# Kernel tuning notes

Hardware: AMD Instinct MI355X
Metric: run time of the kernel (lower is better)

## Reference

```python
import jax, jax.numpy as jnp
import numpy as np

N_NODES = 50000
N_EDGES = 800000
D_IN = 64
D_HID = 256
BN_EPS = 1e-5


def setup_inputs() -> dict:
    key = jax.random.key(0)
    ks = jax.random.split(key, 8)
    s = 1.0 / np.sqrt(D_IN)
    sg = 1.0 / np.sqrt(D_HID)
    return {
        "xs": jax.random.normal(ks[0], (N_NODES, D_IN), jnp.float32),
        "edge_index": jax.random.randint(ks[1], (2, N_EDGES), 0, N_NODES, jnp.int64),
        "W_gcn": jax.random.normal(ks[2], (D_IN, D_HID), jnp.float32) * s,
        "b_gcn": jnp.zeros((D_HID,), jnp.float32),
        "W_lin": jax.random.normal(ks[3], (D_IN, D_HID), jnp.float32) * s,
        "b_lin": jnp.zeros((D_HID,), jnp.float32),
        "W_gate": jax.random.normal(ks[4], (D_HID, D_HID), jnp.float32) * sg,
        "b_gate": jnp.zeros((D_HID,), jnp.float32),
        "bn_gamma": jnp.ones((D_HID,), jnp.float32),
        "bn_beta": jnp.zeros((D_HID,), jnp.float32),
    }


def reference(xs, edge_index, W_gcn, b_gcn, W_lin, b_lin, W_gate, b_gate, bn_gamma, bn_beta):
    N = xs.shape[0]
    # --- GCNConv: add self loops, symmetric normalization D^-1/2 (A+I) D^-1/2 ---
    loops = jnp.arange(N, dtype=edge_index.dtype)
    src = jnp.concatenate([edge_index[0], loops])  # message sources
    dst = jnp.concatenate([edge_index[1], loops])  # aggregation targets
    deg = jax.ops.segment_sum(jnp.ones(src.shape, jnp.float32), dst, num_segments=N)
    dinv = jax.lax.rsqrt(jnp.maximum(deg, 1.0))  # deg >= 1 due to self loops
    norm = dinv[src] * dinv[dst]                 # [E+N]
    h = xs @ W_gcn                               # [N, D_HID]
    z = jax.ops.segment_sum(h[src] * norm[:, None], dst, num_segments=N) + b_gcn
    z = jnp.tanh(z)
    # --- gating + linear residual ---
    g = jax.nn.sigmoid(z @ W_gate + b_gate)
    xl = xs @ W_lin + b_lin
    out = jax.nn.relu((1.0 - g) * xl + g * z)
    # --- BatchNorm over nodes (training-mode batch statistics) ---
    mu = out.mean(axis=0)
    var = out.var(axis=0)
    out = (out - mu) * jax.lax.rsqrt(var + BN_EPS) * bn_gamma + bn_beta
    # dropout is identity in eval mode
    return out
```

## Files before the change

### kernel.cpp

```cpp
#include <hip/hip_runtime.h>
#include <math.h>

#define NN 50000
#define NE 800000
#define D_IN 64
#define D_HID 256
#define BN_EPS 1e-5f
#define ZSTR 264
#define SB 128
#define BCAP 64
#define BINCAP 8192

typedef __attribute__((ext_vector_type(8))) short short8;
typedef __attribute__((ext_vector_type(4))) float f32x4;
typedef __attribute__((ext_vector_type(4))) int int4v;
typedef __attribute__((ext_vector_type(4))) float float4v;

static __device__ __forceinline__ unsigned short f2bf(float f) {
    unsigned int u = __builtin_bit_cast(unsigned int, f);
    u += 0x7FFFu + ((u >> 16) & 1u);
    return (unsigned short)(u >> 16);
}
static __device__ __forceinline__ float bf2f(unsigned short s) {
    unsigned int u = ((unsigned int)s) << 16;
    return __builtin_bit_cast(float, u);
}
static __device__ __forceinline__ float fast_sigmoid(float x) {
    return __builtin_amdgcn_rcpf(1.0f + __expf(-x));
}
static __device__ __forceinline__ float fast_tanh(float x) {
    return 1.0f - 2.0f * __builtin_amdgcn_rcpf(__expf(2.0f * x) + 1.0f);
}

static __device__ __forceinline__ long a_addr(int i, int k) {
    return ((long)((i >> 4) * 2 + (k >> 5)) << 9) + ((((k >> 3) & 3) * 16 + (i & 15)) << 3) + (k & 7);
}

__global__ __launch_bounds__(256) void k_pre(const float* __restrict__ W_gcn,
                      const float* __restrict__ W_lin, const float* __restrict__ W_gate,
                      unsigned short* __restrict__ Wp_gcn, unsigned short* __restrict__ Wp_lin,
                      unsigned short* __restrict__ Wp_gate,
                      const int* __restrict__ eidx, int* __restrict__ bincur,
                      unsigned int* __restrict__ binbuf, int E) {
    int idx = blockIdx.x * blockDim.x + threadIdx.x;
    if (idx < 98304) {
        const float* W;
        unsigned short* Wp;
        int KC, o;
        if (idx < 16384)      { W = W_gcn;  Wp = Wp_gcn;  KC = 2; o = idx; }
        else if (idx < 32768) { W = W_lin;  Wp = Wp_lin;  KC = 2; o = idx - 16384; }
        else                  { W = W_gate; Wp = Wp_gate; KC = 8; o = idx - 32768; }
        int j = o & 7;
        int lane = (o >> 3) & 63;
        int rest = o >> 9;
        int kc = rest % KC;
        int ct = rest / KC;
        int col = ct * 16 + (lane & 15);
        int k = kc * 32 + (lane >> 4) * 8 + j;
        Wp[o] = f2bf(W[k * D_HID + col]);
    }

    int b = blockIdx.x;
    int t = threadIdx.x;
    int nbb = (E + 4095) >> 12;
    if (b < nbb) {
        __shared__ int bcnt[256];
        __shared__ int gbase[256];
        bcnt[t] = 0;
        __syncthreads();
        unsigned int pair[4][4];
        int bin[4][4], lr[4][4];
        bool val[4];
#pragma unroll
        for (int c = 0; c < 4; c++) {
            int e0 = b * 4096 + c * 1024 + t * 4;
            val[c] = e0 < E;
            if (val[c]) {
                int4v s = __builtin_nontemporal_load((const int4v*)(eidx + e0));
                int4v d = __builtin_nontemporal_load((const int4v*)(eidx + E + e0));
                int ss[4] = {s[0], s[1], s[2], s[3]};
                int dd[4] = {d[0], d[1], d[2], d[3]};
#pragma unroll
                for (int j = 0; j < 4; j++) {
                    int bi = dd[j] >> 8;
                    bin[c][j] = bi;
                    pair[c][j] = ((unsigned int)(dd[j] & 255) << 16) | (unsigned int)ss[j];
                    lr[c][j] = atomicAdd(&bcnt[bi], 1);
                }
            }
        }
        __syncthreads();
        if (bcnt[t] > 0) gbase[t] = atomicAdd(&bincur[t], bcnt[t]);
        __syncthreads();
#pragma unroll
        for (int c = 0; c < 4; c++)
            if (val[c]) {
#pragma unroll
                for (int j = 0; j < 4; j++) {
                    int slot = gbase[bin[c][j]] + lr[c][j];
                    if (slot < BINCAP)
                        binbuf[((long)bin[c][j] << 13) + slot] = pair[c][j];
                }
            }
    }
}

__global__ __launch_bounds__(256) void k_binfill(const unsigned int* __restrict__ binbuf,
                      const int* __restrict__ bincur, const float* __restrict__ xs,
                      unsigned short* __restrict__ csr, int* __restrict__ cnt,
                      float* __restrict__ dinv, unsigned short* __restrict__ xscaled,
                      unsigned short* __restrict__ xs_p, int n) {
    __shared__ unsigned short buck[256 * BCAP];
    __shared__ int lcnt[256];
    int b = blockIdx.x;
    int t = threadIdx.x;
    lcnt[t] = 0;
    __syncthreads();
    int tot = bincur[b];
    tot = tot < BINCAP ? tot : BINCAP;
    for (int i = t; i < tot; i += 256) {
        unsigned int p = binbuf[((long)b << 13) + i];
        int dl = p >> 16;
        int src = p & 0xFFFF;
        int r = atomicAdd(&lcnt[dl], 1);
        if (r < BCAP) buck[dl * BCAP + r] = (unsigned short)src;
    }
    __syncthreads();
    int node0 = b << 8;
    if (node0 + t < n) cnt[node0 + t] = lcnt[t];
#pragma unroll
    for (int v = 0; v < 8; v++) {
        int e = (v * 256 + t) * 8;
        int node = e >> 6;
        if (node0 + node < n)
            *(short8*)(csr + ((long)(node0 + node) << 6) + (e & 63)) = *(const short8*)(&buck[e]);
    }
#pragma unroll
    for (int v = 0; v < 8; v++) {
        int item = v * 256 + t;
        int nl = item >> 3;
        int sub = item & 7;
        int node = node0 + nl;
        if (node < n) {
            float dv = rsqrtf(1.0f + (float)lcnt[nl]);
            if (sub == 0) dinv[node] = dv;
            const float* p = xs + (long)node * D_IN + sub * 8;
            float4v f0 = __builtin_nontemporal_load((const float4v*)p);
            float4v f1 = __builtin_nontemporal_load((const float4v*)(p + 4));
            float vals[8] = {f0[0], f0[1], f0[2], f0[3], f1[0], f1[1], f1[2], f1[3]};
            short8 xsc, xsb;
#pragma unroll
            for (int j = 0; j < 8; j++) {
                xsc[j] = (short)f2bf(vals[j] * dv);
                xsb[j] = (short)f2bf(vals[j]);
            }
            *(short8*)(xscaled + (long)node * D_IN + sub * 8) = xsc;
            *(short8*)(xs_p + a_addr(node, sub * 8)) = xsb;
        } else if (node == n) {
            short8 zv = (short8){0, 0, 0, 0, 0, 0, 0, 0};
            *(short8*)(xscaled + (long)n * D_IN + sub * 8) = zv;
        }
    }
}

__global__ __launch_bounds__(256) void k_gather(const unsigned short* __restrict__ csr,
                                                const int* __restrict__ cnt,
                                                const unsigned short* __restrict__ xscaled,
                                                const float* __restrict__ dinv,
                                                unsigned short* __restrict__ agg_p, int n) {
    int wv = threadIdx.x >> 6;
    int lane = threadIdx.x & 63;
    int sub = lane & 7;
    int grp = lane >> 3;
    int i = blockIdx.x * 4 + wv;
    if (i >= n) return;
    int c = cnt[i];
    c = c < BCAP ? c : BCAP;
    float acc[8];
#pragma unroll
    for (int j = 0; j < 8; j++) acc[j] = 0.f;
    int idxv = (lane < c) ? (int)csr[((long)i << 6) + lane] : 0;
    int tmax = (c + 7) >> 3;
    for (int t = 0; t < tmax; t++) {
        int e = t * 8 + grp;
        int rowv = __shfl(idxv, e);
        int row = (e < c) ? rowv : n;
        short8 v = *(const short8*)(xscaled + (long)row * D_IN + sub * 8);
#pragma unroll
        for (int j = 0; j < 8; j++) acc[j] += bf2f((unsigned short)v[j]);
    }
#pragma unroll
    for (int d = 8; d <= 32; d <<= 1)
#pragma unroll
        for (int j = 0; j < 8; j++) acc[j] += __shfl_xor(acc[j], d);
    if (grp == 0) {
        float dv = dinv[i];
        short8 sv = *(const short8*)(xscaled + (long)i * D_IN + sub * 8);
        short8 o;
#pragma unroll
        for (int j = 0; j < 8; j++)
            o[j] = (short)f2bf((acc[j] + bf2f((unsigned short)sv[j])) * dv);
        *(short8*)(agg_p + a_addr(i, sub * 8)) = o;
    }
}

__global__ __launch_bounds__(256) void k_fused(const unsigned short* __restrict__ agg_p,
                        const unsigned short* __restrict__ xs_p,
                        const unsigned short* __restrict__ Wp_gcn,
                        const unsigned short* __restrict__ Wp_lin,
                        const unsigned short* __restrict__ Wp_gate,
                        const float* __restrict__ b_gcn,
                        const float* __restrict__ bg,
                        const float* __restrict__ bl,
                        unsigned short* __restrict__ out_pre,
                        int n) {
    __shared__ unsigned short z_lds[32 * ZSTR];

    int tid = threadIdx.x;
    int wv = tid >> 6;
    int lane = tid & 63;
    int l15 = lane & 15;
    int quad = lane >> 4;
    int rt0 = blockIdx.x * 2;

    short8 aggf[2][2], xsf[2][2];
#pragma unroll
    for (int r = 0; r < 2; r++)
#pragma unroll
        for (int kc = 0; kc < 2; kc++) {
            aggf[r][kc] = *(const short8*)(agg_p + ((long)((rt0 + r) * 2 + kc) << 9) + lane * 8);
            xsf[r][kc]  = *(const short8*)(xs_p  + ((long)((rt0 + r) * 2 + kc) << 9) + lane * 8);
        }

    {
        short8 wg[2][4];
#pragma unroll
        for (int kc = 0; kc < 2; kc++)
#pragma unroll
            for (int tn = 0; tn < 4; tn++)
                wg[kc][tn] = *(const short8*)(Wp_gcn + ((long)((wv * 4 + tn) * 2 + kc) << 9) + lane * 8);
        float bias[4];
#pragma unroll
        for (int tn = 0; tn < 4; tn++) bias[tn] = b_gcn[wv * 64 + tn * 16 + l15];
#pragma unroll
        for (int r = 0; r < 2; r++) {
            f32x4 accz[4];
#pragma unroll
            for (int c = 0; c < 4; c++) accz[c] = (f32x4){0.f, 0.f, 0.f, 0.f};
#pragma unroll
            for (int kc = 0; kc < 2; kc++)
#pragma unroll
                for (int tn = 0; tn < 4; tn++)
                    accz[tn] = __builtin_amdgcn_mfma_f32_16x16x32_bf16(aggf[r][kc], wg[kc][tn], accz[tn], 0, 0, 0);
#pragma unroll
            for (int tn = 0; tn < 4; tn++) {
                int col = wv * 64 + tn * 16 + l15;
#pragma unroll
                for (int r2 = 0; r2 < 4; r2++)
                    z_lds[(r * 16 + quad * 4 + r2) * ZSTR + col] = f2bf(fast_tanh(accz[tn][r2] + bias[tn]));
            }
        }
    }
    __syncthreads();

    uint2 o_pk[2][4];
    float bgc[4], blc[4];
#pragma unroll
    for (int tn = 0; tn < 4; tn++) {
        int col = wv * 64 + tn * 16 + l15;
        bgc[tn] = bg[col];
        blc[tn] = bl[col];
    }
#pragma unroll
    for (int tnp = 0; tnp < 2; tnp++) {
        f32x4 accl[2][2];
#pragma unroll
        for (int r = 0; r < 2; r++)
#pragma unroll
            for (int h = 0; h < 2; h++) accl[r][h] = (f32x4){0.f, 0.f, 0.f, 0.f};
#pragma unroll
        for (int kc = 0; kc < 2; kc++) {
            short8 wl0 = *(const short8*)(Wp_lin + ((long)((wv * 4 + tnp * 2 + 0) * 2 + kc) << 9) + lane * 8);
            short8 wl1 = *(const short8*)(Wp_lin + ((long)((wv * 4 + tnp * 2 + 1) * 2 + kc) << 9) + lane * 8);
#pragma unroll
            for (int r = 0; r < 2; r++) {
                accl[r][0] = __builtin_amdgcn_mfma_f32_16x16x32_bf16(xsf[r][kc], wl0, accl[r][0], 0, 0, 0);
                accl[r][1] = __builtin_amdgcn_mfma_f32_16x16x32_bf16(xsf[r][kc], wl1, accl[r][1], 0, 0, 0);
            }
        }
        f32x4 acc1[2][2];
#pragma unroll
        for (int r = 0; r < 2; r++)
#pragma unroll
            for (int h = 0; h < 2; h++) acc1[r][h] = (f32x4){0.f, 0.f, 0.f, 0.f};
#pragma unroll
        for (int kc = 0; kc < 8; kc++) {
            short8 w0 = *(const short8*)(Wp_gate + ((long)((wv * 4 + tnp * 2 + 0) * 8 + kc) << 9) + lane * 8);
            short8 w1 = *(const short8*)(Wp_gate + ((long)((wv * 4 + tnp * 2 + 1) * 8 + kc) << 9) + lane * 8);
#pragma unroll
            for (int r = 0; r < 2; r++) {
                short8 af = *(const short8*)(&z_lds[(r * 16 + l15) * ZSTR + kc * 32 + quad * 8]);
                acc1[r][0] = __builtin_amdgcn_mfma_f32_16x16x32_bf16(af, w0, acc1[r][0], 0, 0, 0);
                acc1[r][1] = __builtin_amdgcn_mfma_f32_16x16x32_bf16(af, w1, acc1[r][1], 0, 0, 0);
            }
        }
#pragma unroll
        for (int h = 0; h < 2; h++) {
            int tn = tnp * 2 + h;
            int col = wv * 64 + tn * 16 + l15;
#pragma unroll
            for (int r = 0; r < 2; r++) {
                unsigned short op4[4];
#pragma unroll
                for (int r2 = 0; r2 < 4; r2++) {
                    int rl = r * 16 + quad * 4 + r2;
                    float g = fast_sigmoid(acc1[r][h][r2] + bgc[tn]);
                    float zv = bf2f(z_lds[rl * ZSTR + col]);
                    float xv = accl[r][h][r2] + blc[tn];
                    float o = fmaxf((1.f - g) * xv + g * zv, 0.f);
                    op4[r2] = f2bf(o);
                }
                o_pk[r][tn].x = (unsigned int)op4[0] | ((unsigned int)op4[1] << 16);
                o_pk[r][tn].y = (unsigned int)op4[2] | ((unsigned int)op4[3] << 16);
            }
        }
    }
    __syncthreads();

#pragma unroll
    for (int r = 0; r < 2; r++)
#pragma unroll
        for (int tn = 0; tn < 4; tn++) {
            int col = wv * 64 + tn * 16 + l15;
            int rl = r * 16 + quad * 4;
            z_lds[(rl + 0) * ZSTR + col] = (unsigned short)(o_pk[r][tn].x & 0xFFFF);
            z_lds[(rl + 1) * ZSTR + col] = (unsigned short)(o_pk[r][tn].x >> 16);
            z_lds[(rl + 2) * ZSTR + col] = (unsigned short)(o_pk[r][tn].y & 0xFFFF);
            z_lds[(rl + 3) * ZSTR + col] = (unsigned short)(o_pk[r][tn].y >> 16);
        }
    __syncthreads();

#pragma unroll
    for (int it = 0; it < 4; it++) {
        int g = it * 2048 + tid * 8;
        int row = g >> 8;
        int col = g & 255;
        short8 v = *(const short8*)(&z_lds[row * ZSTR + col]);
        *(short8*)(out_pre + (long)(blockIdx.x * 32 + row) * D_HID + col) = v;
    }
    (void)n;
}

__global__ __launch_bounds__(256) void k_stats(const unsigned short* __restrict__ op,
                        float* __restrict__ colsum, float* __restrict__ colsumsq, int n) {
    __shared__ float reds[4][32][8];
    __shared__ float redq[4][32][8];
    int tid = threadIdx.x;
    int wv = tid >> 6;
    int lane = tid & 63;
    int cg = tid & 31;
    int rb = tid >> 5;
    float ls[8], lq[8];
#pragma unroll
    for (int j = 0; j < 8; j++) { ls[j] = 0.f; lq[j] = 0.f; }
    for (int row = blockIdx.x * 8 + rb; row < n; row += SB * 8) {
        short8 v = *(const short8*)(op + (long)row * D_HID + cg * 8);
#pragma unroll
        for (int j = 0; j < 8; j++) {
            float f = bf2f((unsigned short)v[j]);
            ls[j] += f;
            lq[j] += f * f;
        }
    }
#pragma unroll
    for (int j = 0; j < 8; j++) {
        ls[j] += __shfl_xor(ls[j], 32);
        lq[j] += __shfl_xor(lq[j], 32);
    }
    if (lane < 32) {
#pragma unroll
        for (int j = 0; j < 8; j++) {
            reds[wv][cg][j] = ls[j];
            redq[wv][cg][j] = lq[j];
        }
    }
    __syncthreads();
    if (wv == 0 && lane < 32) {
#pragma unroll
        for (int j = 0; j < 8; j++) {
            float s = reds[0][cg][j] + reds[1][cg][j] + reds[2][cg][j] + reds[3][cg][j];
            float q = redq[0][cg][j] + redq[1][cg][j] + redq[2][cg][j] + redq[3][cg][j];
            atomicAdd(&colsum[cg * 8 + j], s);
            atomicAdd(&colsumsq[cg * 8 + j], q);
        }
    }
}

__global__ __launch_bounds__(256) void k_bn_apply(const unsigned short* __restrict__ op,
                           float* __restrict__ out,
                           const float* __restrict__ colsum, const float* __restrict__ colsumsq,
                           const float* __restrict__ gamma, const float* __restrict__ beta,
                           int n, int total8) {
    int i8 = blockIdx.x * blockDim.x + threadIdx.x;
    if (i8 >= total8) return;
    long idx = (long)i8 * 8;
    short8 p = *(const short8*)(op + idx);
    int c = (int)(idx & (D_HID - 1));
    float inv_n = 1.0f / (float)n;
    float vo[8];
#pragma unroll
    for (int j = 0; j < 8; j++) {
        float mu = colsum[c + j] * inv_n;
        float var = colsumsq[c + j] * inv_n - mu * mu;
        float sc = gamma[c + j] * rsqrtf(var + BN_EPS);
        vo[j] = bf2f((unsigned short)p[j]) * sc + (beta[c + j] - mu * sc);
    }
    float4v v0 = {vo[0], vo[1], vo[2], vo[3]};
    float4v v1 = {vo[4], vo[5], vo[6], vo[7]};
    __builtin_nontemporal_store(v0, (float4v*)(out + idx));
    __builtin_nontemporal_store(v1, (float4v*)(out + idx + 4));
}

extern "C" void kernel_launch(void* const* d_in, const int* in_sizes, int n_in,
                              void* d_out, int out_size, void* d_ws, size_t ws_size,
                              hipStream_t stream) {
    const float* xs     = (const float*)d_in[0];
    const int*   eidx   = (const int*)d_in[1];
    const float* W_gcn  = (const float*)d_in[2];
    const float* b_gcn  = (const float*)d_in[3];
    const float* W_lin  = (const float*)d_in[4];
    const float* b_lin  = (const float*)d_in[5];
    const float* W_gate = (const float*)d_in[6];
    const float* b_gate = (const float*)d_in[7];
    const float* gamma  = (const float*)d_in[8];
    const float* beta   = (const float*)d_in[9];
    float* out = (float*)d_out;

    const int n = in_sizes[0] / D_IN;
    const int E = in_sizes[1] / 2;
    const int npad = (n + 63) & ~63;
    const int nbins = (n + 255) >> 8;

    char* ws = (char*)d_ws;
    size_t off = 0;
    auto alloc = [&](size_t bytes) {
        char* p = ws + off;
        off += (bytes + 511) & ~(size_t)511;
        return p;
    };
    size_t zero_begin = off;
    int*            bincur   = (int*)alloc(256 * 4);
    float*          colsum   = (float*)alloc(D_HID * 4);
    float*          colsumsq = (float*)alloc(D_HID * 4);
    size_t zero_end = off;
    int*            cnt      = (int*)alloc((size_t)n * 4);
    unsigned int*   binbuf   = (unsigned int*)alloc((size_t)nbins * BINCAP * 4);
    unsigned short* csr      = (unsigned short*)alloc((size_t)n * BCAP * 2);
    float*          dinv     = (float*)alloc((size_t)n * 4);
    unsigned short* xscaled  = (unsigned short*)alloc((size_t)(n + 1) * D_IN * 2);
    unsigned short* xs_p     = (unsigned short*)alloc((size_t)npad * D_IN * 2);
    unsigned short* agg_p    = (unsigned short*)alloc((size_t)npad * D_IN * 2);
    unsigned short* out_pre  = (unsigned short*)alloc((size_t)npad * D_HID * 2);
    unsigned short* Wp_gcn   = (unsigned short*)alloc((size_t)D_IN * D_HID * 2);
    unsigned short* Wp_lin   = (unsigned short*)alloc((size_t)D_IN * D_HID * 2);
    unsigned short* Wp_gate  = (unsigned short*)alloc((size_t)D_HID * D_HID * 2);
    (void)ws_size;

    const int B = 256;

    hipMemsetAsync(ws + zero_begin, 0, zero_end - zero_begin, stream);
    k_pre<<<384, B, 0, stream>>>(W_gcn, W_lin, W_gate, Wp_gcn, Wp_lin, Wp_gate,
                                 eidx, bincur, binbuf, E);
    k_binfill<<<nbins, B, 0, stream>>>(binbuf, bincur, xs, csr, cnt, dinv, xscaled, xs_p, n);
    k_gather<<<(n + 3) / 4, B, 0, stream>>>(csr, cnt, xscaled, dinv, agg_p, n);
    k_fused<<<npad / 32, B, 0, stream>>>(agg_p, xs_p, Wp_gcn, Wp_lin, Wp_gate,
                                         b_gcn, b_gate, b_lin, out_pre, n);
    k_stats<<<SB, B, 0, stream>>>(out_pre, colsum, colsumsq, n);
    {
        int total8 = n * D_HID / 8;
        k_bn_apply<<<(total8 + B - 1) / B, B, 0, stream>>>(out_pre, out, colsum, colsumsq,
                                                           gamma, beta, n, total8);
    }
}
```

Baseline: 214.9 us.

## Fuse all stages into one cooperative persistent kernel with grid syncs

Result: slower. 481.8 us (+124.2%).

```diff
diff --git a/kernel.cpp b/kernel.cpp
--- a/kernel.cpp
+++ b/kernel.cpp
@@ -1,5 +1,8 @@
 #include <hip/hip_runtime.h>
+#include <hip/hip_cooperative_groups.h>
 #include <math.h>
+
+namespace cg = cooperative_groups;
 
 #define NN 50000
 #define NE 800000
@@ -10,6 +13,7 @@
 #define SB 128
 #define BCAP 64
 #define BINCAP 8192
+#define SMEM_BYTES 33792
 
 typedef __attribute__((ext_vector_type(8))) short short8;
 typedef __attribute__((ext_vector_type(4))) float f32x4;
@@ -36,389 +40,394 @@
     return ((long)((i >> 4) * 2 + (k >> 5)) << 9) + ((((k >> 3) & 3) * 16 + (i & 15)) << 3) + (k & 7);
 }
 
-__global__ __launch_bounds__(256) void k_pre(const float* __restrict__ W_gcn,
-                      const float* __restrict__ W_lin, const float* __restrict__ W_gate,
-                      unsigned short* __restrict__ Wp_gcn, unsigned short* __restrict__ Wp_lin,
-                      unsigned short* __restrict__ Wp_gate,
-                      const int* __restrict__ eidx, int* __restrict__ bincur,
-                      unsigned int* __restrict__ binbuf, int E) {
-    int idx = blockIdx.x * blockDim.x + threadIdx.x;
-    if (idx < 98304) {
-        const float* W;
-        unsigned short* Wp;
-        int KC, o;
-        if (idx < 16384)      { W = W_gcn;  Wp = Wp_gcn;  KC = 2; o = idx; }
-        else if (idx < 32768) { W = W_lin;  Wp = Wp_lin;  KC = 2; o = idx - 16384; }
-        else                  { W = W_gate; Wp = Wp_gate; KC = 8; o = idx - 32768; }
-        int j = o & 7;
-        int lane = (o >> 3) & 63;
-        int rest = o >> 9;
-        int kc = rest % KC;
-        int ct = rest / KC;
-        int col = ct * 16 + (lane & 15);
-        int k = kc * 32 + (lane >> 4) * 8 + j;
-        Wp[o] = f2bf(W[k * D_HID + col]);
-    }
-
-    int b = blockIdx.x;
-    int t = threadIdx.x;
-    int nbb = (E + 4095) >> 12;
-    if (b < nbb) {
-        __shared__ int bcnt[256];
-        __shared__ int gbase[256];
-        bcnt[t] = 0;
-        __syncthreads();
-        unsigned int pair[4][4];
-        int bin[4][4], lr[4][4];
-        bool val[4];
-#pragma unroll
-        for (int c = 0; c < 4; c++) {
-            int e0 = b * 4096 + c * 1024 + t * 4;
-            val[c] = e0 < E;
-            if (val[c]) {
-                int4v s = __builtin_nontemporal_load((const int4v*)(eidx + e0));
-                int4v d = __builtin_nontemporal_load((const int4v*)(eidx + E + e0));
-                int ss[4] = {s[0], s[1], s[2], s[3]};
-                int dd[4] = {d[0], d[1], d[2], d[3]};
-#pragma unroll
-                for (int j = 0; j < 4; j++) {
-                    int bi = dd[j] >> 8;
-                    bin[c][j] = bi;
-                    pair[c][j] = ((unsigned int)(dd[j] & 255) << 16) | (unsigned int)ss[j];
-                    lr[c][j] = atomicAdd(&bcnt[bi], 1);
-                }
-            }
-        }
-        __syncthreads();
-        if (bcnt[t] > 0) gbase[t] = atomicAdd(&bincur[t], bcnt[t]);
-        __syncthreads();
-#pragma unroll
-        for (int c = 0; c < 4; c++)
-            if (val[c]) {
-#pragma unroll
-                for (int j = 0; j < 4; j++) {
-                    int slot = gbase[bin[c][j]] + lr[c][j];
-                    if (slot < BINCAP)
-                        binbuf[((long)bin[c][j] << 13) + slot] = pair[c][j];
-                }
-            }
-    }
-}
-
-__global__ __launch_bounds__(256) void k_binfill(const unsigned int* __restrict__ binbuf,
-                      const int* __restrict__ bincur, const float* __restrict__ xs,
-                      unsigned short* __restrict__ csr, int* __restrict__ cnt,
-                      float* __restrict__ dinv, unsigned short* __restrict__ xscaled,
-                      unsigned short* __restrict__ xs_p, int n) {
-    __shared__ unsigned short buck[256 * BCAP];
-    __shared__ int lcnt[256];
-    int b = blockIdx.x;
-    int t = threadIdx.x;
-    lcnt[t] = 0;
-    __syncthreads();
-    int tot = bincur[b];
-    tot = tot < BINCAP ? tot : BINCAP;
-    for (int i = t; i < tot; i += 256) {
-        unsigned int p = binbuf[((long)b << 13) + i];
-        int dl = p >> 16;
-        int src = p & 0xFFFF;
-        int r = atomicAdd(&lcnt[dl], 1);
-        if (r < BCAP) buck[dl * BCAP + r] = (unsigned short)src;
-    }
-    __syncthreads();
-    int node0 = b << 8;
-    if (node0 + t < n) cnt[node0 + t] = lcnt[t];
-#pragma unroll
-    for (int v = 0; v < 8; v++) {
-        int e = (v * 256 + t) * 8;
-        int node = e >> 6;
-        if (node0 + node < n)
-            *(short8*)(csr + ((long)(node0 + node) << 6) + (e & 63)) = *(const short8*)(&buck[e]);
-    }
-#pragma unroll
-    for (int v = 0; v < 8; v++) {
-        int item = v * 256 + t;
-        int nl = item >> 3;
-        int sub = item & 7;
-        int node = node0 + nl;
-        if (node < n) {
-            float dv = rsqrtf(1.0f + (float)lcnt[nl]);
-            if (sub == 0) dinv[node] = dv;
-            const float* p = xs + (long)node * D_IN + sub * 8;
-            float4v f0 = __builtin_nontemporal_load((const float4v*)p);
-            float4v f1 = __builtin_nontemporal_load((const float4v*)(p + 4));
-            float vals[8] = {f0[0], f0[1], f0[2], f0[3], f1[0], f1[1], f1[2], f1[3]};
-            short8 xsc, xsb;
-#pragma unroll
-            for (int j = 0; j < 8; j++) {
-                xsc[j] = (short)f2bf(vals[j] * dv);
-                xsb[j] = (short)f2bf(vals[j]);
-            }
-            *(short8*)(xscaled + (long)node * D_IN + sub * 8) = xsc;
-            *(short8*)(xs_p + a_addr(node, sub * 8)) = xsb;
-        } else if (node == n) {
-            short8 zv = (short8){0, 0, 0, 0, 0, 0, 0, 0};
-            *(short8*)(xscaled + (long)n * D_IN + sub * 8) = zv;
-        }
-    }
-}
-
-__global__ __launch_bounds__(256) void k_gather(const unsigned short* __restrict__ csr,
-                                                const int* __restrict__ cnt,
-                                                const unsigned short* __restrict__ xscaled,
-                                                const float* __restrict__ dinv,
-                                                unsigned short* __restrict__ agg_p, int n) {
-    int wv = threadIdx.x >> 6;
-    int lane = threadIdx.x & 63;
-    int sub = lane & 7;
-    int grp = lane >> 3;
-    int i = blockIdx.x * 4 + wv;
-    if (i >= n) return;
-    int c = cnt[i];
-    c = c < BCAP ? c : BCAP;
-    float acc[8];
-#pragma unroll
-    for (int j = 0; j < 8; j++) acc[j] = 0.f;
-    int idxv = (lane < c) ? (int)csr[((long)i << 6) + lane] : 0;
-    int tmax = (c + 7) >> 3;
-    for (int t = 0; t < tmax; t++) {
-        int e = t * 8 + grp;
-        int rowv = __shfl(idxv, e);
-        int row = (e < c) ? rowv : n;
-        short8 v = *(const short8*)(xscaled + (long)row * D_IN + sub * 8);
-#pragma unroll
-        for (int j = 0; j < 8; j++) acc[j] += bf2f((unsigned short)v[j]);
-    }
-#pragma unroll
-    for (int d = 8; d <= 32; d <<= 1)
-#pragma unroll
-        for (int j = 0; j < 8; j++) acc[j] += __shfl_xor(acc[j], d);
-    if (grp == 0) {
-        float dv = dinv[i];
-        short8 sv = *(const short8*)(xscaled + (long)i * D_IN + sub * 8);
-        short8 o;
-#pragma unroll
-        for (int j = 0; j < 8; j++)
-            o[j] = (short)f2bf((acc[j] + bf2f((unsigned short)sv[j])) * dv);
-        *(short8*)(agg_p + a_addr(i, sub * 8)) = o;
-    }
-}
-
-__global__ __launch_bounds__(256) void k_fused(const unsigned short* __restrict__ agg_p,
-                        const unsigned short* __restrict__ xs_p,
-                        const unsigned short* __restrict__ Wp_gcn,
-                        const unsigned short* __restrict__ Wp_lin,
-                        const unsigned short* __restrict__ Wp_gate,
-                        const float* __restrict__ b_gcn,
-                        const float* __restrict__ bg,
-                        const float* __restrict__ bl,
-                        unsigned short* __restrict__ out_pre,
-                        int n) {
-    __shared__ unsigned short z_lds[32 * ZSTR];
-
-    int tid = threadIdx.x;
-    int wv = tid >> 6;
-    int lane = tid & 63;
-    int l15 = lane & 15;
-    int quad = lane >> 4;
-    int rt0 = blockIdx.x * 2;
-
-    short8 aggf[2][2], xsf[2][2];
-#pragma unroll
-    for (int r = 0; r < 2; r++)
-#pragma unroll
-        for (int kc = 0; kc < 2; kc++) {
-            aggf[r][kc] = *(const short8*)(agg_p + ((long)((rt0 + r) * 2 + kc) << 9) + lane * 8);
-            xsf[r][kc]  = *(const short8*)(xs_p  + ((long)((rt0 + r) * 2 + kc) << 9) + lane * 8);
-        }
-
-    {
-        short8 wg[2][4];
-#pragma unroll
-        for (int kc = 0; kc < 2; kc++)
-#pragma unroll
-            for (int tn = 0; tn < 4; tn++)
-                wg[kc][tn] = *(const short8*)(Wp_gcn + ((long)((wv * 4 + tn) * 2 + kc) << 9) + lane * 8);
-        float bias[4];
-#pragma unroll
-        for (int tn = 0; tn < 4; tn++) bias[tn] = b_gcn[wv * 64 + tn * 16 + l15];
-#pragma unroll
-        for (int r = 0; r < 2; r++) {
-            f32x4 accz[4];
-#pragma unroll
-            for (int c = 0; c < 4; c++) accz[c] = (f32x4){0.f, 0.f, 0.f, 0.f};
-#pragma unroll
-            for (int kc = 0; kc < 2; kc++)
-#pragma unroll
-                for (int tn = 0; tn < 4; tn++)
-                    accz[tn] = __builtin_amdgcn_mfma_f32_16x16x32_bf16(aggf[r][kc], wg[kc][tn], accz[tn], 0, 0, 0);
+__global__ __launch_bounds__(256) void k_mega(
+        const float* __restrict__ xs, const int* __restrict__ eidx,
+        const float* __restrict__ W_gcn, const float* __restrict__ b_gcn,
+        const float* __restrict__ W_lin, const float* __restrict__ b_lin,
+        const float* __restrict__ W_gate, const float* __restrict__ b_gate,
+        const float* __restrict__ gamma, const float* __restrict__ beta,
+        float* __restrict__ out,
+        int* __restrict__ bincur, float* __restrict__ colsum, float* __restrict__ colsumsq,
+        int* __restrict__ cnt, unsigned int* __restrict__ binbuf,
+        unsigned short* __restrict__ csr, float* __restrict__ dinv,
+        unsigned short* __restrict__ xscaled, unsigned short* __restrict__ xs_p,
+        unsigned short* __restrict__ agg_p, unsigned short* __restrict__ out_pre,
+        unsigned short* __restrict__ Wp_gcn, unsigned short* __restrict__ Wp_lin,
+        unsigned short* __restrict__ Wp_gate,
+        int n, int E) {
+    cg::grid_group grid = cg::this_grid();
+    __shared__ __align__(16) char smem[SMEM_BYTES];
+    const int G = gridDim.x;
+    const int bid = blockIdx.x;
+    const int t = threadIdx.x;
+
+    if (bid == 0) bincur[t] = 0;
+    if (bid == 1) { colsum[t] = 0.f; colsumsq[t] = 0.f; }
+    grid.sync();
+
+    {
+        int* bcnt = (int*)smem;
+        int* gbase = (int*)(smem + 1024);
+        int nbb = (E + 4095) >> 12;
+        for (int b = bid; b < nbb; b += G) {
+            bcnt[t] = 0;
+            __syncthreads();
+            unsigned int pair[4][4];
+            int bin[4][4], lr[4][4];
+            bool val[4];
+#pragma unroll
+            for (int c = 0; c < 4; c++) {
+                int e0 = b * 4096 + c * 1024 + t * 4;
+                val[c] = e0 < E;
+                if (val[c]) {
+                    int4v s = __builtin_nontemporal_load((const int4v*)(eidx + e0));
+                    int4v d = __builtin_nontemporal_load((const int4v*)(eidx + E + e0));
+                    int ss[4] = {s[0], s[1], s[2], s[3]};
+                    int dd[4] = {d[0], d[1], d[2], d[3]};
+#pragma unroll
+                    for (int j = 0; j < 4; j++) {
+                        int bi = dd[j] >> 8;
+                        bin[c][j] = bi;
+                        pair[c][j] = ((unsigned int)(dd[j] & 255) << 16) | (unsigned int)ss[j];
+                        lr[c][j] = atomicAdd(&bcnt[bi], 1);
+                    }
+                }
+            }
+            __syncthreads();
+            if (bcnt[t] > 0) gbase[t] = atomicAdd(&bincur[t], bcnt[t]);
+            __syncthreads();
+#pragma unroll
+            for (int c = 0; c < 4; c++)
+                if (val[c])
+#pragma unroll
+                    for (int j = 0; j < 4; j++) {
+                        int slot = gbase[bin[c][j]] + lr[c][j];
+                        if (slot < BINCAP)
+                            binbuf[((long)bin[c][j] << 13) + slot] = pair[c][j];
+                    }
+            __syncthreads();
+        }
+        for (int idx = bid * 256 + t; idx < 98304; idx += G * 256) {
+            const float* W;
+            unsigned short* Wp;
+            int KC, o;
+            if (idx < 16384)      { W = W_gcn;  Wp = Wp_gcn;  KC = 2; o = idx; }
+            else if (idx < 32768) { W = W_lin;  Wp = Wp_lin;  KC = 2; o = idx - 16384; }
+            else                  { W = W_gate; Wp = Wp_gate; KC = 8; o = idx - 32768; }
+            int j = o & 7;
+            int lane = (o >> 3) & 63;
+            int rest = o >> 9;
+            int kc = rest % KC;
+            int ct = rest / KC;
+            int col = ct * 16 + (lane & 15);
+            int k = kc * 32 + (lane >> 4) * 8 + j;
+            Wp[o] = f2bf(W[k * D_HID + col]);
+        }
+    }
+    grid.sync();
+
+    {
+        unsigned short* buck = (unsigned short*)smem;
+        int* lcnt = (int*)(smem + 32768);
+        int nbins = (n + 255) >> 8;
+        for (int b = bid; b < nbins; b += G) {
+            lcnt[t] = 0;
+            __syncthreads();
+            int tot = bincur[b];
+            tot = tot < BINCAP ? tot : BINCAP;
+            for (int i2 = t; i2 < tot; i2 += 256) {
+                unsigned int p = binbuf[((long)b << 13) + i2];
+                int dl = p >> 16;
+                int src = p & 0xFFFF;
+                int r = atomicAdd(&lcnt[dl], 1);
+                if (r < BCAP) buck[dl * BCAP + r] = (unsigned short)src;
+            }
+            __syncthreads();
+            int node0 = b << 8;
+            if (node0 + t < n) cnt[node0 + t] = lcnt[t];
+#pragma unroll
+            for (int v = 0; v < 8; v++) {
+                int e = (v * 256 + t) * 8;
+                int node = e >> 6;
+                if (node0 + node < n)
+                    *(short8*)(csr + ((long)(node0 + node) << 6) + (e & 63)) = *(const short8*)(&buck[e]);
+            }
+#pragma unroll
+            for (int v = 0; v < 8; v++) {
+                int item = v * 256 + t;
+                int nl = item >> 3;
+                int sub = item & 7;
+                int node = node0 + nl;
+                if (node < n) {
+                    float dv = rsqrtf(1.0f + (float)lcnt[nl]);
+                    if (sub == 0) dinv[node] = dv;
+                    const float* p = xs + (long)node * D_IN + sub * 8;
+                    float4v f0 = __builtin_nontemporal_load((const float4v*)p);
+                    float4v f1 = __builtin_nontemporal_load((const float4v*)(p + 4));
+                    float vals[8] = {f0[0], f0[1], f0[2], f0[3], f1[0], f1[1], f1[2], f1[3]};
+                    short8 xsc, xsb;
+#pragma unroll
+                    for (int j = 0; j < 8; j++) {
+                        xsc[j] = (short)f2bf(vals[j] * dv);
+                        xsb[j] = (short)f2bf(vals[j]);
+                    }
+                    *(short8*)(xscaled + (long)node * D_IN + sub * 8) = xsc;
+                    *(short8*)(xs_p + a_addr(node, sub * 8)) = xsb;
+                } else if (node == n) {
+                    short8 zv = (short8){0, 0, 0, 0, 0, 0, 0, 0};
+                    *(short8*)(xscaled + (long)n * D_IN + sub * 8) = zv;
+                }
+            }
+            __syncthreads();
+        }
+    }
+    grid.sync();
+
+    {
+        int wv = t >> 6;
+        int lane = t & 63;
+        int sub = lane & 7;
+        int grp = lane >> 3;
+        for (int i = bid * 4 + wv; i < n; i += G * 4) {
+            int c = cnt[i];
+            c = c < BCAP ? c : BCAP;
+            float acc[8];
+#pragma unroll
+            for (int j = 0; j < 8; j++) acc[j] = 0.f;
+            int idxv = (lane < c) ? (int)csr[((long)i << 6) + lane] : 0;
+            int tmax = (c + 7) >> 3;
+            for (int tt = 0; tt < tmax; tt++) {
+                int e = tt * 8 + grp;
+                int rowv = __shfl(idxv, e);
+                int row = (e < c) ? rowv : n;
+                short8 v = *(const short8*)(xscaled + (long)row * D_IN + sub * 8);
+#pragma unroll
+                for (int j = 0; j < 8; j++) acc[j] += bf2f((unsigned short)v[j]);
+            }
+#pragma unroll
+            for (int d = 8; d <= 32; d <<= 1)
+#pragma unroll
+                for (int j = 0; j < 8; j++) acc[j] += __shfl_xor(acc[j], d);
+            if (grp == 0) {
+                float dv = dinv[i];
+                short8 sv = *(const short8*)(xscaled + (long)i * D_IN + sub * 8);
+                short8 o;
+#pragma unroll
+                for (int j = 0; j < 8; j++)
+                    o[j] = (short)f2bf((acc[j] + bf2f((unsigned short)sv[j])) * dv);
+                *(short8*)(agg_p + a_addr(i, sub * 8)) = o;
+            }
+        }
+    }
+    grid.sync();
+
+    {
+        unsigned short* z_lds = (unsigned short*)smem;
+        int wv = t >> 6;
+        int lane = t & 63;
+        int l15 = lane & 15;
+        int quad = lane >> 4;
+        int ntile = ((n + 63) & ~63) / 32;
+        for (int bt = bid; bt < ntile; bt += G) {
+            int rt0 = bt * 2;
+            __syncthreads();
+
+            short8 aggf[2][2], xsf[2][2];
+#pragma unroll
+            for (int r = 0; r < 2; r++)
+#pragma unroll
+                for (int kc = 0; kc < 2; kc++) {
+                    aggf[r][kc] = *(const short8*)(agg_p + ((long)((rt0 + r) * 2 + kc) << 9) + lane * 8);
+                    xsf[r][kc]  = *(const short8*)(xs_p  + ((long)((rt0 + r) * 2 + kc) << 9) + lane * 8);
+                }
+
+            {
+                short8 wg[2][4];
+#pragma unroll
+                for (int kc = 0; kc < 2; kc++)
+#pragma unroll
+                    for (int tn = 0; tn < 4; tn++)
+                        wg[kc][tn] = *(const short8*)(Wp_gcn + ((long)((wv * 4 + tn) * 2 + kc) << 9) + lane * 8);
+                float bias[4];
+#pragma unroll
+                for (int tn = 0; tn < 4; tn++) bias[tn] = b_gcn[wv * 64 + tn * 16 + l15];
+#pragma unroll
+                for (int r = 0; r < 2; r++) {
+                    f32x4 accz[4];
+#pragma unroll
+                    for (int c = 0; c < 4; c++) accz[c] = (f32x4){0.f, 0.f, 0.f, 0.f};
+#pragma unroll
+                    for (int kc = 0; kc < 2; kc++)
+#pragma unroll
+                        for (int tn = 0; tn < 4; tn++)
+                            accz[tn] = __builtin_amdgcn_mfma_f32_16x16x32_bf16(aggf[r][kc], wg[kc][tn], accz[tn], 0, 0, 0);
+#pragma unroll
+                    for (int tn = 0; tn < 4; tn++) {
+                        int col = wv * 64 + tn * 16 + l15;
+#pragma unroll
+                        for (int r2 = 0; r2 < 4; r2++)
+                            z_lds[(r * 16 + quad * 4 + r2) * ZSTR + col] = f2bf(fast_tanh(accz[tn][r2] + bias[tn]));
+                    }
+                }
+            }
+            __syncthreads();
+
+            uint2 o_pk[2][4];
+            float bgc[4], blc[4];
 #pragma unroll
             for (int tn = 0; tn < 4; tn++) {
                 int col = wv * 64 + tn * 16 + l15;
-#pragma unroll
-                for (int r2 = 0; r2 < 4; r2++)
-                    z_lds[(r * 16 + quad * 4 + r2) * ZSTR + col] = f2bf(fast_tanh(accz[tn][r2] + bias[tn]));
-            }
-        }
-    }
-    __syncthreads();
-
-    uint2 o_pk[2][4];
-    float bgc[4], blc[4];
-#pragma unroll
-    for (int tn = 0; tn < 4; tn++) {
-        int col = wv * 64 + tn * 16 + l15;
-        bgc[tn] = bg[col];
-        blc[tn] = bl[col];
-    }
-#pragma unroll
-    for (int tnp = 0; tnp < 2; tnp++) {
-        f32x4 accl[2][2];
-#pragma unroll
-        for (int r = 0; r < 2; r++)
-#pragma unroll
-            for (int h = 0; h < 2; h++) accl[r][h] = (f32x4){0.f, 0.f, 0.f, 0.f};
-#pragma unroll
-        for (int kc = 0; kc < 2; kc++) {
-            short8 wl0 = *(const short8*)(Wp_lin + ((long)((wv * 4 + tnp * 2 + 0) * 2 + kc) << 9) + lane * 8);
-            short8 wl1 = *(const short8*)(Wp_lin + ((long)((wv * 4 + tnp * 2 + 1) * 2 + kc) << 9) + lane * 8);
-#pragma unroll
-            for (int r = 0; r < 2; r++) {
-                accl[r][0] = __builtin_amdgcn_mfma_f32_16x16x32_bf16(xsf[r][kc], wl0, accl[r][0], 0, 0, 0);
-                accl[r][1] = __builtin_amdgcn_mfma_f32_16x16x32_bf16(xsf[r][kc], wl1, accl[r][1], 0, 0, 0);
-            }
-        }
-        f32x4 acc1[2][2];
-#pragma unroll
-        for (int r = 0; r < 2; r++)
-#pragma unroll
-            for (int h = 0; h < 2; h++) acc1[r][h] = (f32x4){0.f, 0.f, 0.f, 0.f};
-#pragma unroll
-        for (int kc = 0; kc < 8; kc++) {
-            short8 w0 = *(const short8*)(Wp_gate + ((long)((wv * 4 + tnp * 2 + 0) * 8 + kc) << 9) + lane * 8);
-            short8 w1 = *(const short8*)(Wp_gate + ((long)((wv * 4 + tnp * 2 + 1) * 8 + kc) << 9) + lane * 8);
-#pragma unroll
-            for (int r = 0; r < 2; r++) {
-                short8 af = *(const short8*)(&z_lds[(r * 16 + l15) * ZSTR + kc * 32 + quad * 8]);
-                acc1[r][0] = __builtin_amdgcn_mfma_f32_16x16x32_bf16(af, w0, acc1[r][0], 0, 0, 0);
-                acc1[r][1] = __builtin_amdgcn_mfma_f32_16x16x32_bf16(af, w1, acc1[r][1], 0, 0, 0);
-            }
-        }
-#pragma unroll
-        for (int h = 0; h < 2; h++) {
-            int tn = tnp * 2 + h;
-            int col = wv * 64 + tn * 16 + l15;
-#pragma unroll
-            for (int r = 0; r < 2; r++) {
-                unsigned short op4[4];
-#pragma unroll
-                for (int r2 = 0; r2 < 4; r2++) {
-                    int rl = r * 16 + quad * 4 + r2;
-                    float g = fast_sigmoid(acc1[r][h][r2] + bgc[tn]);
-                    float zv = bf2f(z_lds[rl * ZSTR + col]);
-                    float xv = accl[r][h][r2] + blc[tn];
-                    float o = fmaxf((1.f - g) * xv + g * zv, 0.f);
-                    op4[r2] = f2bf(o);
-                }
-                o_pk[r][tn].x = (unsigned int)op4[0] | ((unsigned int)op4[1] << 16);
-                o_pk[r][tn].y = (unsigned int)op4[2] | ((unsigned int)op4[3] << 16);
-            }
-        }
-    }
-    __syncthreads();
-
-#pragma unroll
-    for (int r = 0; r < 2; r++)
-#pragma unroll
-        for (int tn = 0; tn < 4; tn++) {
-            int col = wv * 64 + tn * 16 + l15;
-            int rl = r * 16 + quad * 4;
-            z_lds[(rl + 0) * ZSTR + col] = (unsigned short)(o_pk[r][tn].x & 0xFFFF);
-            z_lds[(rl + 1) * ZSTR + col] = (unsigned short)(o_pk[r][tn].x >> 16);
-            z_lds[(rl + 2) * ZSTR + col] = (unsigned short)(o_pk[r][tn].y & 0xFFFF);
-            z_lds[(rl + 3) * ZSTR + col] = (unsigned short)(o_pk[r][tn].y >> 16);
-        }
-    __syncthreads();
-
-#pragma unroll
-    for (int it = 0; it < 4; it++) {
-        int g = it * 2048 + tid * 8;
-        int row = g >> 8;
-        int col = g & 255;
-        short8 v = *(const short8*)(&z_lds[row * ZSTR + col]);
-        *(short8*)(out_pre + (long)(blockIdx.x * 32 + row) * D_HID + col) = v;
-    }
-    (void)n;
-}
-
-__global__ __launch_bounds__(256) void k_stats(const unsigned short* __restrict__ op,
-                        float* __restrict__ colsum, float* __restrict__ colsumsq, int n) {
-    __shared__ float reds[4][32][8];
-    __shared__ float redq[4][32][8];
-    int tid = threadIdx.x;
-    int wv = tid >> 6;
-    int lane = tid & 63;
-    int cg = tid & 31;
-    int rb = tid >> 5;
-    float ls[8], lq[8];
-#pragma unroll
-    for (int j = 0; j < 8; j++) { ls[j] = 0.f; lq[j] = 0.f; }
-    for (int row = blockIdx.x * 8 + rb; row < n; row += SB * 8) {
-        short8 v = *(const short8*)(op + (long)row * D_HID + cg * 8);
-#pragma unroll
-        for (int j = 0; j < 8; j++) {
-            float f = bf2f((unsigned short)v[j]);
-            ls[j] += f;
-            lq[j] += f * f;
-        }
-    }
-#pragma unroll
-    for (int j = 0; j < 8; j++) {
-        ls[j] += __shfl_xor(ls[j], 32);
-        lq[j] += __shfl_xor(lq[j], 32);
-    }
-    if (lane < 32) {
-#pragma unroll
-        for (int j = 0; j < 8; j++) {
-            reds[wv][cg][j] = ls[j];
-            redq[wv][cg][j] = lq[j];
-        }
-    }
-    __syncthreads();
-    if (wv == 0 && lane < 32) {
-#pragma unroll
-        for (int j = 0; j < 8; j++) {
-            float s = reds[0][cg][j] + reds[1][cg][j] + reds[2][cg][j] + reds[3][cg][j];
-            float q = redq[0][cg][j] + redq[1][cg][j] + redq[2][cg][j] + redq[3][cg][j];
-            atomicAdd(&colsum[cg * 8 + j], s);
-            atomicAdd(&colsumsq[cg * 8 + j], q);
-        }
-    }
-}
-
-__global__ __launch_bounds__(256) void k_bn_apply(const unsigned short* __restrict__ op,
-                           float* __restrict__ out,
-                           const float* __restrict__ colsum, const float* __restrict__ colsumsq,
-                           const float* __restrict__ gamma, const float* __restrict__ beta,
-                           int n, int total8) {
-    int i8 = blockIdx.x * blockDim.x + threadIdx.x;
-    if (i8 >= total8) return;
-    long idx = (long)i8 * 8;
-    short8 p = *(const short8*)(op + idx);
-    int c = (int)(idx & (D_HID - 1));
-    float inv_n = 1.0f / (float)n;
-    float vo[8];
-#pragma unroll
-    for (int j = 0; j < 8; j++) {
-        float mu = colsum[c + j] * inv_n;
-        float var = colsumsq[c + j] * inv_n - mu * mu;
-        float sc = gamma[c + j] * rsqrtf(var + BN_EPS);
-        vo[j] = bf2f((unsigned short)p[j]) * sc + (beta[c + j] - mu * sc);
-    }
-    float4v v0 = {vo[0], vo[1], vo[2], vo[3]};
-    float4v v1 = {vo[4], vo[5], vo[6], vo[7]};
-    __builtin_nontemporal_store(v0, (float4v*)(out + idx));
-    __builtin_nontemporal_store(v1, (float4v*)(out + idx + 4));
+                bgc[tn] = b_gate[col];
+                blc[tn] = b_lin[col];
+            }
+#pragma unroll
+            for (int tnp = 0; tnp < 2; tnp++) {
+                f32x4 accl[2][2];
+#pragma unroll
+                for (int r = 0; r < 2; r++)
+#pragma unroll
+                    for (int h = 0; h < 2; h++) accl[r][h] = (f32x4){0.f, 0.f, 0.f, 0.f};
+#pragma unroll
+                for (int kc = 0; kc < 2; kc++) {
+                    short8 wl0 = *(const short8*)(Wp_lin + ((long)((wv * 4 + tnp * 2 + 0) * 2 + kc) << 9) + lane * 8);
+                    short8 wl1 = *(const short8*)(Wp_lin + ((long)((wv * 4 + tnp * 2 + 1) * 2 + kc) << 9) + lane * 8);
+#pragma unroll
+                    for (int r = 0; r < 2; r++) {
+                        accl[r][0] = __builtin_amdgcn_mfma_f32_16x16x32_bf16(xsf[r][kc], wl0, accl[r][0], 0, 0, 0);
+                        accl[r][1] = __builtin_amdgcn_mfma_f32_16x16x32_bf16(xsf[r][kc], wl1, accl[r][1], 0, 0, 0);
+                    }
+                }
+                f32x4 acc1[2][2];
+#pragma unroll
+                for (int r = 0; r < 2; r++)
+#pragma unroll
+                    for (int h = 0; h < 2; h++) acc1[r][h] = (f32x4){0.f, 0.f, 0.f, 0.f};
+#pragma unroll
+                for (int kc = 0; kc < 8; kc++) {
+                    short8 w0 = *(const short8*)(Wp_gate + ((long)((wv * 4 + tnp * 2 + 0) * 8 + kc) << 9) + lane * 8);
+                    short8 w1 = *(const short8*)(Wp_gate + ((long)((wv * 4 + tnp * 2 + 1) * 8 + kc) << 9) + lane * 8);
+#pragma unroll
+                    for (int r = 0; r < 2; r++) {
+                        short8 af = *(const short8*)(&z_lds[(r * 16 + l15) * ZSTR + kc * 32 + quad * 8]);
+                        acc1[r][0] = __builtin_amdgcn_mfma_f32_16x16x32_bf16(af, w0, acc1[r][0], 0, 0, 0);
+                        acc1[r][1] = __builtin_amdgcn_mfma_f32_16x16x32_bf16(af, w1, acc1[r][1], 0, 0, 0);
+                    }
+                }
+#pragma unroll
+                for (int h = 0; h < 2; h++) {
+                    int tn = tnp * 2 + h;
+                    int col = wv * 64 + tn * 16 + l15;
+#pragma unroll
+                    for (int r = 0; r < 2; r++) {
+                        unsigned short op4[4];
+#pragma unroll
+                        for (int r2 = 0; r2 < 4; r2++) {
+                            int rl = r * 16 + quad * 4 + r2;
+                            float g = fast_sigmoid(acc1[r][h][r2] + bgc[tn]);
+                            float zv = bf2f(z_lds[rl * ZSTR + col]);
+                            float xv = accl[r][h][r2] + blc[tn];
+                            float o = fmaxf((1.f - g) * xv + g * zv, 0.f);
+                            op4[r2] = f2bf(o);
+                        }
+                        o_pk[r][tn].x = (unsigned int)op4[0] | ((unsigned int)op4[1] << 16);
+                        o_pk[r][tn].y = (unsigned int)op4[2] | ((unsigned int)op4[3] << 16);
+                    }
+                }
+            }
+            __syncthreads();
+
+#pragma unroll
+            for (int r = 0; r < 2; r++)
+#pragma unroll
+                for (int tn = 0; tn < 4; tn++) {
+                    int col = wv * 64 + tn * 16 + l15;
+                    int rl = r * 16 + quad * 4;
+                    z_lds[(rl + 0) * ZSTR + col] = (unsigned short)(o_pk[r][tn].x & 0xFFFF);
+                    z_lds[(rl + 1) * ZSTR + col] = (unsigned short)(o_pk[r][tn].x >> 16);
+                    z_lds[(rl + 2) * ZSTR + col] = (unsigned short)(o_pk[r][tn].y & 0xFFFF);
+                    z_lds[(rl + 3) * ZSTR + col] = (unsigned short)(o_pk[r][tn].y >> 16);
+                }
+            __syncthreads();
+
+#pragma unroll
+            for (int it = 0; it < 4; it++) {
+                int g = it * 2048 + t * 8;
+                int row = g >> 8;
+                int col = g & 255;
+                short8 v = *(const short8*)(&z_lds[row * ZSTR + col]);
+                *(short8*)(out_pre + (long)(bt * 32 + row) * D_HID + col) = v;
+            }
+        }
+    }
+    grid.sync();
+
+    {
+        if (bid < SB) {
+            float (*reds)[32][8] = (float(*)[32][8])smem;
+            float (*redq)[32][8] = (float(*)[32][8])(smem + 4096);
+            int wv = t >> 6;
+            int lane = t & 63;
+            int cgc = t & 31;
+            int rb = t >> 5;
+            float ls[8], lq[8];
+#pragma unroll
+            for (int j = 0; j < 8; j++) { ls[j] = 0.f; lq[j] = 0.f; }
+            for (int row = bid * 8 + rb; row < n; row += SB * 8) {
+                short8 v = *(const short8*)(out_pre + (long)row * D_HID + cgc * 8);
+#pragma unroll
+                for (int j = 0; j < 8; j++) {
+                    float f = bf2f((unsigned short)v[j]);
+                    ls[j] += f;
+                    lq[j] += f * f;
+                }
+            }
+#pragma unroll
+            for (int j = 0; j < 8; j++) {
+                ls[j] += __shfl_xor(ls[j], 32);
+                lq[j] += __shfl_xor(lq[j], 32);
+            }
+            if (lane < 32) {
+#pragma unroll
+                for (int j = 0; j < 8; j++) {
+                    reds[wv][cgc][j] = ls[j];
+                    redq[wv][cgc][j] = lq[j];
+                }
+            }
+            __syncthreads();
+            if (wv == 0 && lane < 32) {
+#pragma unroll
+                for (int j = 0; j < 8; j++) {
+                    float s = reds[0][cgc][j] + reds[1][cgc][j] + reds[2][cgc][j] + reds[3][cgc][j];
+                    float q = redq[0][cgc][j] + redq[1][cgc][j] + redq[2][cgc][j] + redq[3][cgc][j];
+                    atomicAdd(&colsum[cgc * 8 + j], s);
+                    atomicAdd(&colsumsq[cgc * 8 + j], q);
+                }
+            }
+        }
+    }
+    grid.sync();
+
+    {
+        int total8 = n * D_HID / 8;
+        float inv_n = 1.0f / (float)n;
+        for (int i8 = bid * 256 + t; i8 < total8; i8 += G * 256) {
+            long idx = (long)i8 * 8;
+            short8 p = *(const short8*)(out_pre + idx);
+            int c = (int)(idx & (D_HID - 1));
+            float vo[8];
+#pragma unroll
+            for (int j = 0; j < 8; j++) {
+                float mu = colsum[c + j] * inv_n;
+                float var = colsumsq[c + j] * inv_n - mu * mu;
+                float sc = gamma[c + j] * rsqrtf(var + BN_EPS);
+                vo[j] = bf2f((unsigned short)p[j]) * sc + (beta[c + j] - mu * sc);
+            }
+            float4v v0 = {vo[0], vo[1], vo[2], vo[3]};
+            float4v v1 = {vo[4], vo[5], vo[6], vo[7]};
+            __builtin_nontemporal_store(v0, (float4v*)(out + idx));
+            __builtin_nontemporal_store(v1, (float4v*)(out + idx + 4));
+        }
+    }
 }
 
 extern "C" void kernel_launch(void* const* d_in, const int* in_sizes, int n_in,
@@ -436,8 +445,8 @@
     const float* beta   = (const float*)d_in[9];
     float* out = (float*)d_out;
 
-    const int n = in_sizes[0] / D_IN;
-    const int E = in_sizes[1] / 2;
+    int n = in_sizes[0] / D_IN;
+    int E = in_sizes[1] / 2;
     const int npad = (n + 63) & ~63;
     const int nbins = (n + 255) >> 8;
 
@@ -448,11 +457,9 @@
         off += (bytes + 511) & ~(size_t)511;
         return p;
     };
-    size_t zero_begin = off;
     int*            bincur   = (int*)alloc(256 * 4);
     float*          colsum   = (float*)alloc(D_HID * 4);
     float*          colsumsq = (float*)alloc(D_HID * 4);
-    size_t zero_end = off;
     int*            cnt      = (int*)alloc((size_t)n * 4);
     unsigned int*   binbuf   = (unsigned int*)alloc((size_t)nbins * BINCAP * 4);
     unsigned short* csr      = (unsigned short*)alloc((size_t)n * BCAP * 2);
@@ -466,19 +473,19 @@
     unsigned short* Wp_gate  = (unsigned short*)alloc((size_t)D_HID * D_HID * 2);
     (void)ws_size;
 
-    const int B = 256;
-
-    hipMemsetAsync(ws + zero_begin, 0, zero_end - zero_begin, stream);
-    k_pre<<<384, B, 0, stream>>>(W_gcn, W_lin, W_gate, Wp_gcn, Wp_lin, Wp_gate,
-                                 eidx, bincur, binbuf, E);
-    k_binfill<<<nbins, B, 0, stream>>>(binbuf, bincur, xs, csr, cnt, dinv, xscaled, xs_p, n);
-    k_gather<<<(n + 3) / 4, B, 0, stream>>>(csr, cnt, xscaled, dinv, agg_p, n);
-    k_fused<<<npad / 32, B, 0, stream>>>(agg_p, xs_p, Wp_gcn, Wp_lin, Wp_gate,
-                                         b_gcn, b_gate, b_lin, out_pre, n);
-    k_stats<<<SB, B, 0, stream>>>(out_pre, colsum, colsumsq, n);
-    {
-        int total8 = n * D_HID / 8;
-        k_bn_apply<<<(total8 + B - 1) / B, B, 0, stream>>>(out_pre, out, colsum, colsumsq,
-                                                           gamma, beta, n, total8);
-    }
-}
+    static int bpc = 0;
+    if (bpc == 0) {
+        if (hipOccupancyMaxActiveBlocksPerMultiprocessor(&bpc, k_mega, 256, 0) != hipSuccess
+            || bpc < 1)
+            bpc = 1;
+    }
+    int G = bpc * 256;
+    if (G > 2048) G = 2048;
+
+    void* args[] = { &xs, &eidx, &W_gcn, &b_gcn, &W_lin, &b_lin, &W_gate, &b_gate,
+                     &gamma, &beta, &out,
+                     &bincur, &colsum, &colsumsq, &cnt, &binbuf, &csr, &dinv,
+                     &xscaled, &xs_p, &agg_p, &out_pre,
+                     &Wp_gcn, &Wp_lin, &Wp_gate, &n, &E };
+    hipLaunchCooperativeKernel((const void*)k_mega, dim3(G), dim3(256), args, 0, stream);
+}
```
